# Optimization experiments

Hardware: AMD Instinct MI355X
Metric: run time of the kernel (lower is better)

The kernel has to match this reference:

```python
import jax, jax.numpy as jnp
import numpy as np

N, E, B = 100000, 640000, 2000
NODE_TYPES, EDGE_TYPES = 16, 5
ND, ED, EMB, L = 256, 128, 256, 3  # node_dim, edge_dim, emb_dim, num encoder blocks


def setup_inputs() -> dict:
    key = jax.random.key(0)
    ks = jax.random.split(key, 20)
    s = 0.02
    inp = {
        "h_node": jax.random.normal(ks[0], (N, NODE_TYPES), jnp.float32),
        "pos_node": jax.random.normal(ks[1], (N, 3), jnp.float32),
        "h_edge": jax.random.normal(ks[2], (E, EDGE_TYPES), jnp.float32),
        "W_node": jax.random.normal(ks[3], (NODE_TYPES, ND), jnp.float32) * s,
        "W_edge": jax.random.normal(ks[4], (EDGE_TYPES, ED), jnp.float32) * s,
        # per-block encoder params (stacked over L blocks)
        "W_eu": jax.random.normal(ks[5], (L, ED + 2 * ND + 1, ED), jnp.float32) * s,
        "b_eu": jnp.zeros((L, ED), jnp.float32),
        "W_msg": jax.random.normal(ks[6], (L, ND + ED, ND), jnp.float32) * s,
        "b_msg": jnp.zeros((L, ND), jnp.float32),
        "W_nu": jax.random.normal(ks[7], (L, 2 * ND, ND), jnp.float32) * s,
        "b_nu": jnp.zeros((L, ND), jnp.float32),
        # final MLP: in=ND+ED, hidden=2*EMB, out=EMB (num_layer=2)
        "Wf1": jax.random.normal(ks[8], (ND + ED, 2 * EMB), jnp.float32) * s,
        "bf1": jnp.zeros((2 * EMB,), jnp.float32),
        "Wf2": jax.random.normal(ks[9], (2 * EMB, EMB), jnp.float32) * s,
        "bf2": jnp.zeros((EMB,), jnp.float32),
        "edge_index": jax.random.randint(ks[10], (2, E), 0, N, jnp.int64),
        "batch_node": jnp.sort(jax.random.randint(ks[11], (N,), 0, B, jnp.int64)),
        "batch_edge": jnp.sort(jax.random.randint(ks[12], (E,), 0, B, jnp.int64)),
    }
    return inp


def _segment_mean(x, ids, num_segments):
    tot = jax.ops.segment_sum(x, ids, num_segments=num_segments)
    cnt = jax.ops.segment_sum(jnp.ones((x.shape[0], 1), x.dtype), ids,
                              num_segments=num_segments)
    return tot / jnp.maximum(cnt, 1.0)


def reference(h_node, pos_node, h_edge, W_node, W_edge, W_eu, b_eu,
              W_msg, b_msg, W_nu, b_nu, Wf1, bf1, Wf2, bf2,
              edge_index, batch_node, batch_edge):
    src, dst = edge_index[0], edge_index[1]
    # embed node / edge type features
    hn = h_node @ W_node            # [N, ND]
    he = h_edge @ W_edge            # [E, ED]
    # NodeEdgeNet: L message-passing blocks with geometric edge feature
    dist = jnp.linalg.norm(pos_node[dst] - pos_node[src], axis=-1,
                           keepdims=True)  # [E, 1]
    for l in range(L):
        e_in = jnp.concatenate([he, hn[src], hn[dst], dist], axis=-1)
        he = jax.nn.relu(e_in @ W_eu[l] + b_eu[l])                 # edge update
        msg = jax.nn.relu(jnp.concatenate([hn[src], he], axis=-1)
                          @ W_msg[l] + b_msg[l])                    # [E, ND]
        agg = jax.ops.segment_sum(msg, dst, num_segments=N)         # [N, ND]
        hn = hn + jax.nn.relu(jnp.concatenate([hn, agg], axis=-1)
                              @ W_nu[l] + b_nu[l])                  # node update
    # per-graph mean pooling (replaces python loop over k with segment mean)
    mean_n = _segment_mean(hn, batch_node, B)   # [B, ND]
    mean_e = _segment_mean(he, batch_edge, B)   # [B, ED]
    h_sub = jnp.concatenate([mean_n, mean_e], axis=-1)  # [B, ND+ED]
    emb = jax.nn.relu(h_sub @ Wf1 + bf1) @ Wf2 + bf2     # [B, EMB]
    return emb, batch_node
```

## Files before the change

kernel.cpp:

```cpp
#include <hip/hip_runtime.h>
#include <hip/hip_bf16.h>
#include <math.h>

#define NN 100000
#define NE 640000
#define NB 2000

typedef __attribute__((ext_vector_type(4))) float v4f;
typedef long long ll64;
#define MFMA8(a, b, c) __builtin_amdgcn_mfma_f32_16x16x32_fp8_fp8(a, b, c, 0, 0, 0)

#define INV_S 0.000244140625f
#define ASCL 16.0f
#define AINV 0.0625f

#if __has_builtin(__builtin_amdgcn_cvt_pk_fp8_f32) && __has_builtin(__builtin_amdgcn_cvt_f32_fp8)
#define HW_FP8 1
#else
#define HW_FP8 0
#endif

__device__ __forceinline__ int IDX(const void* p, size_t i, int is64) {
    return is64 ? (int)((const long long*)p)[i] : ((const int*)p)[i];
}
__device__ __forceinline__ int clampi(int v, int n) {
    return ((unsigned)v < (unsigned)n) ? v : 0;
}

__global__ void k_detect(const int* bn32, int* flag) {
    if (threadIdx.x == 0 && blockIdx.x == 0) {
        int is64 = 1;
        for (int k = 50001; k < 50401; k += 2)
            if (bn32[k] != 0) { is64 = 0; break; }
        *flag = is64;
    }
}

__device__ __forceinline__ unsigned sw_enc_fp8(float x) {
    unsigned s = (__float_as_uint(x) >> 24) & 0x80u;
    float ax = fminf(fabsf(x), 448.f);
    if (ax < 0.015625f) {
        unsigned m = (unsigned)(ax * 512.f + 0.5f);
        return s | m;
    }
    unsigned b = __float_as_uint(ax) + 0x00080000u;
    unsigned e = (b >> 23) - 120u;
    unsigned m = (b >> 20) & 7u;
    unsigned v = (e << 3) | m;
    if (v > 0x7Eu) v = 0x7Eu;
    return s | v;
}
__device__ __forceinline__ float sw_dec_fp8(unsigned b) {
    unsigned s = (b & 0x80u) << 24;
    unsigned e = (b >> 3) & 15u;
    unsigned m = b & 7u;
    if (e) return __uint_as_float(s | ((e + 120u) << 23) | (m << 20));
    float f = (float)m * 0.001953125f;
    return (b & 0x80u) ? -f : f;
}
__device__ __forceinline__ unsigned enc1(float x) {
#if HW_FP8
    return (unsigned)__builtin_amdgcn_cvt_pk_fp8_f32(x, x, 0, false) & 255u;
#else
    return sw_enc_fp8(x);
#endif
}
__device__ __forceinline__ unsigned encpk(float a, float b) {
#if HW_FP8
    return (unsigned)__builtin_amdgcn_cvt_pk_fp8_f32(a, b, 0, false) & 0xFFFFu;
#else
    return sw_enc_fp8(a) | (sw_enc_fp8(b) << 8);
#endif
}
__device__ __forceinline__ float dec1(unsigned b) {
#if HW_FP8
    return __builtin_amdgcn_cvt_f32_fp8((int)b, 0);
#else
    return sw_dec_fp8(b);
#endif
}
__device__ __forceinline__ float bf_f(unsigned short u) {
    return __uint_as_float((unsigned)u << 16);
}
__device__ __forceinline__ unsigned short f_to_bf(float x) {
    __hip_bfloat16 h = __float2bfloat16(x);
    return *(unsigned short*)&h;
}

__global__ __launch_bounds__(256) void k_node_embed(const float* __restrict__ h_node,
                                                    const float* __restrict__ W,
                                                    unsigned char* __restrict__ hn8) {
    __shared__ float sh[8][16];
    int t = threadIdx.x;
    int r0 = blockIdx.x * 8;
    if (t < 128) sh[t >> 4][t & 15] = h_node[r0 * 16 + t];
    float w[16];
#pragma unroll
    for (int k = 0; k < 16; ++k) w[k] = W[k * 256 + t];
    __syncthreads();
#pragma unroll
    for (int r = 0; r < 8; ++r) {
        float acc = 0.f;
#pragma unroll
        for (int k = 0; k < 16; ++k) acc += sh[r][k] * w[k];
        hn8[(size_t)(r0 + r) * 256 + t] = (unsigned char)enc1(ASCL * acc);
    }
}

__global__ __launch_bounds__(256) void k_edge_embed(const float* __restrict__ h_edge,
                                                    const float* __restrict__ W,
                                                    const int* __restrict__ perm,
                                                    unsigned char* __restrict__ he8) {
    __shared__ float sh[16][5];
    int t = threadIdx.x;
    int e0 = blockIdx.x * 16;
    if (t < 80) {
        int row = t / 5, col = t % 5;
        int e = perm[e0 + row];
        sh[row][col] = h_edge[(size_t)e * 5 + col];
    }
    int c = t & 127;
    int es = t >> 7;
    float w[5];
#pragma unroll
    for (int k = 0; k < 5; ++k) w[k] = W[k * 128 + c];
    __syncthreads();
#pragma unroll
    for (int e = 0; e < 8; ++e) {
        int ee = es * 8 + e;
        float acc = 0.f;
#pragma unroll
        for (int k = 0; k < 5; ++k) acc += sh[ee][k] * w[k];
        he8[(size_t)(e0 + ee) * 128 + c] = (unsigned char)enc1(ASCL * acc);
    }
}

__global__ __launch_bounds__(256) void k_tr_w1(const float* __restrict__ W,
                                               unsigned char* __restrict__ WT) {
    int i = blockIdx.x * 256 + threadIdx.x;
    if (i >= 3 * 128 * 128) return;
    int l = i / 16384, r = i % 16384;
    int n = r / 128, k = r % 128;
    WT[i] = (unsigned char)enc1(256.f * W[(size_t)l * 641 * 128 + (size_t)k * 128 + n]);
}
__global__ __launch_bounds__(256) void k_tr_w2(const float* __restrict__ W,
                                               unsigned char* __restrict__ WT) {
    int i = blockIdx.x * 256 + threadIdx.x;
    if (i >= 3 * 256 * 128) return;
    int l = i / 32768, r = i % 32768;
    int n = r / 128, k = r % 128;
    WT[i] = (unsigned char)enc1(256.f * W[(size_t)l * 384 * 256 + (size_t)(256 + k) * 256 + n]);
}
__global__ __launch_bounds__(256) void k_tr_nu(const float* __restrict__ W,
                                               unsigned char* __restrict__ WT) {
    int i = blockIdx.x * 256 + threadIdx.x;
    if (i >= 3 * 256 * 512) return;
    int l = i / 131072, r = i % 131072;
    int n = r / 512, k = r % 512;
    WT[i] = (unsigned char)enc1(256.f * W[(size_t)l * 512 * 256 + (size_t)k * 256 + n]);
}
__global__ __launch_bounds__(256) void k_tr_pre(const float* __restrict__ Weu,
                                                const float* __restrict__ Wmsg,
                                                unsigned char* __restrict__ WT) {
    int i = blockIdx.x * 256 + threadIdx.x;
    if (i >= 3 * 512 * 256) return;
    int l = i / 131072, r = i % 131072;
    int n = r / 256, k = r % 256;
    float w;
    if (n < 128)      w = Weu[(size_t)l * 641 * 128 + (size_t)(128 + k) * 128 + n];
    else if (n < 256) w = Weu[(size_t)l * 641 * 128 + (size_t)(384 + k) * 128 + (n - 128)];
    else              w = Wmsg[(size_t)l * 384 * 256 + (size_t)k * 256 + (n - 256)];
    WT[i] = (unsigned char)enc1(256.f * w);
}

__global__ __launch_bounds__(256) void k_hist(const void* __restrict__ ei,
                                              const int* __restrict__ flag,
                                              int* __restrict__ hist) {
    int e = blockIdx.x * 256 + threadIdx.x;
    if (e >= NE) return;
    int d = clampi(IDX(ei, (size_t)NE + e, *flag), NN);
    atomicAdd(&hist[d], 1);
}
__global__ __launch_bounds__(1024) void k_scan(const int* __restrict__ hist,
                                               int* __restrict__ rowptr) {
    __shared__ int part[1024];
    int t = threadIdx.x;
    const int C = 98;
    int s = 0;
    for (int j = 0; j < C; ++j) {
        int i = t * C + j;
        if (i < NN) s += hist[i];
    }
    part[t] = s;
    __syncthreads();
    if (t == 0) {
        int run = 0;
        for (int i = 0; i < 1024; ++i) { int v = part[i]; part[i] = run; run += v; }
    }
    __syncthreads();
    int run = part[t];
    for (int j = 0; j < C; ++j) {
        int i = t * C + j;
        if (i < NN) { rowptr[i] = run; run += hist[i]; }
    }
}
__global__ __launch_bounds__(256) void k_perm(const void* __restrict__ ei,
                                              const int* __restrict__ flag,
                                              const float* __restrict__ pos,
                                              int* __restrict__ cursor,
                                              int* __restrict__ perm,
                                              int* __restrict__ inv,
                                              int* __restrict__ srcs,
                                              int* __restrict__ dsts,
                                              float* __restrict__ dist_s) {
    int e = blockIdx.x * 256 + threadIdx.x;
    if (e >= NE) return;
    int is64 = *flag;
    int s = clampi(IDX(ei, (size_t)e, is64), NN);
    int d = clampi(IDX(ei, (size_t)NE + e, is64), NN);
    int p = atomicAdd(&cursor[d], 1);
    perm[p] = e;
    inv[e] = p;
    srcs[p] = s;
    dsts[p] = d;
    float dx = pos[d * 3 + 0] - pos[s * 3 + 0];
    float dy = pos[d * 3 + 1] - pos[s * 3 + 1];
    float dz = pos[d * 3 + 2] - pos[s * 3 + 2];
    dist_s[p] = sqrtf(dx * dx + dy * dy + dz * dz);
}

#define NP_AS 264
__global__ __launch_bounds__(256, 3) void k_node_pre(
    const unsigned char* __restrict__ hn8, const unsigned char* __restrict__ WpreT,
    unsigned char* __restrict__ R) {
    __shared__ unsigned char s_A[64 * NP_AS];
    int t = threadIdx.x;
    int rb = blockIdx.x * 64;
    {
        int row = t >> 2, sb = t & 3;
        int gr = rb + row; if (gr >= NN) gr = NN - 1;
        const uint4* sp = (const uint4*)(hn8 + (size_t)gr * 256 + sb * 64);
        uint4 a = sp[0], b = sp[1], c = sp[2], d = sp[3];
        uint4* dp = (uint4*)&s_A[row * NP_AS + sb * 64];
        dp[0] = a; dp[1] = b; dp[2] = c; dp[3] = d;
    }
    __syncthreads();
    int lane = t & 63, wv = t >> 6, quad = lane >> 4, l16 = lane & 15;
    v4f zero4 = {0.f, 0.f, 0.f, 0.f};
#pragma unroll
    for (int pass = 0; pass < 2; ++pass) {
        int nt0 = wv * 8 + pass * 4;
        v4f acc[4][4];
#pragma unroll
        for (int mt = 0; mt < 4; ++mt)
#pragma unroll
            for (int nl = 0; nl < 4; ++nl) acc[mt][nl] = zero4;
#pragma unroll 2
        for (int k = 0; k < 256; k += 32) {
            int ko = k + quad * 8;
            ll64 b[4];
#pragma unroll
            for (int nl = 0; nl < 4; ++nl)
                b[nl] = *(const ll64*)(WpreT + (size_t)((nt0 + nl) * 16 + l16) * 256 + ko);
#pragma unroll
            for (int mt = 0; mt < 4; ++mt) {
                ll64 a = *(const ll64*)&s_A[(mt * 16 + l16) * NP_AS + ko];
#pragma unroll
                for (int nl = 0; nl < 4; ++nl) acc[mt][nl] = MFMA8(a, b[nl], acc[mt][nl]);
            }
        }
#pragma unroll
        for (int nl = 0; nl < 4; ++nl) {
            int c = (nt0 + nl) * 16 + l16;
#pragma unroll
            for (int mt = 0; mt < 4; ++mt)
#pragma unroll
                for (int rr = 0; rr < 2; ++rr) {
                    int rw0 = mt * 16 + quad * 4 + rr * 2;
                    unsigned pk = encpk(acc[mt][nl][rr * 2] * 0.00390625f,
                                        acc[mt][nl][rr * 2 + 1] * 0.00390625f);
                    if (rb + rw0 < NN)
                        R[(size_t)(rb + rw0) * 512 + c] = (unsigned char)(pk & 255u);
                    if (rb + rw0 + 1 < NN)
                        R[(size_t)(rb + rw0 + 1) * 512 + c] = (unsigned char)(pk >> 8);
                }
        }
    }
}

#define EF_S 136
#define EF_QS 264
#define EF_MS 264
__global__ __launch_bounds__(256, 4) void k_edge_fused(
    unsigned char* __restrict__ he8, const unsigned char* __restrict__ R,
    const float* __restrict__ dist_s,
    const int* __restrict__ srcs, const int* __restrict__ dsts,
    const unsigned char* __restrict__ W1T, const float* __restrict__ W_eu,
    const float* __restrict__ b_eu,
    const unsigned char* __restrict__ W2T, const float* __restrict__ b_msg,
    unsigned short* __restrict__ agg) {
    __shared__ __align__(16) unsigned char s_A[32 * EF_S];
    __shared__ __align__(16) unsigned char s_Pd[32 * EF_S];
    __shared__ __align__(16) unsigned char s_Ph[32 * EF_S];
    __shared__ __align__(16) unsigned char s_Q[32 * EF_QS];
    __shared__ __align__(16) unsigned short s_msg[32 * EF_MS];
    __shared__ float s_dist[32];
    __shared__ int s_dsti[32];
    int t = threadIdx.x;
    int eb = blockIdx.x * 32;
    int row = t >> 3, sb = t & 7;
    int sid = srcs[eb + row];
    int did = dsts[eb + row];
    if (t < 32) {
        s_dsti[t] = dsts[eb + t];
        s_dist[t] = dist_s[eb + t];
    }
    *(uint4*)&s_A[row * EF_S + sb * 16] =
        *(const uint4*)(he8 + (size_t)(eb + row) * 128 + sb * 16);
    *(uint4*)&s_Ph[row * EF_S + sb * 16] =
        *(const uint4*)(R + (size_t)sid * 512 + sb * 16);
    *(uint4*)&s_Pd[row * EF_S + sb * 16] =
        *(const uint4*)(R + (size_t)did * 512 + 128 + sb * 16);
    {
        const uint4* qp = (const uint4*)(R + (size_t)sid * 512 + 256 + sb * 32);
        uint4 q0 = qp[0], q1 = qp[1];
        *(uint4*)&s_Q[row * EF_QS + sb * 32] = q0;
        *(uint4*)&s_Q[row * EF_QS + sb * 32 + 16] = q1;
    }
    int lane = t & 63, wv = t >> 6, quad = lane >> 4, l16 = lane & 15;
    int n0 = wv * 2;
    const unsigned char* B0 = W1T + (size_t)(n0 * 16 + l16) * 128 + quad * 8;
    ll64 Brg[4][2];
#pragma unroll
    for (int kk = 0; kk < 4; ++kk) {
        Brg[kk][0] = *(const ll64*)(B0 + kk * 32);
        Brg[kk][1] = *(const ll64*)(B0 + 2048 + kk * 32);
    }
    __syncthreads();

    v4f zero4 = {0.f, 0.f, 0.f, 0.f};
    v4f acc[2][2];
    acc[0][0] = zero4; acc[0][1] = zero4; acc[1][0] = zero4; acc[1][1] = zero4;
#pragma unroll
    for (int kk = 0; kk < 4; ++kk) {
        int ko = kk * 32 + quad * 8;
#pragma unroll
        for (int mt = 0; mt < 2; ++mt) {
            ll64 a = *(const ll64*)&s_A[(mt * 16 + l16) * EF_S + ko];
            acc[mt][0] = MFMA8(a, Brg[kk][0], acc[mt][0]);
            acc[mt][1] = MFMA8(a, Brg[kk][1], acc[mt][1]);
        }
    }
#pragma unroll
    for (int nl = 0; nl < 2; ++nl) {
        int c = (n0 + nl) * 16 + l16;
        float w640 = W_eu[640 * 128 + c];
        float bb = b_eu[c];
#pragma unroll
        for (int mt = 0; mt < 2; ++mt)
#pragma unroll
            for (int rr = 0; rr < 2; ++rr) {
                int rw0 = mt * 16 + quad * 4 + rr * 2;
                int rw1 = rw0 + 1;
                float S0 = (dec1(s_Ph[rw0 * EF_S + c]) +
                            dec1(s_Pd[rw0 * EF_S + c])) * AINV;
                float S1 = (dec1(s_Ph[rw1 * EF_S + c]) +
                            dec1(s_Pd[rw1 * EF_S + c])) * AINV;
                float v0 = fmaxf(acc[mt][nl][rr * 2] * INV_S + S0 +
                                 s_dist[rw0] * w640 + bb, 0.f);
                float v1 = fmaxf(acc[mt][nl][rr * 2 + 1] * INV_S + S1 +
                                 s_dist[rw1] * w640 + bb, 0.f);
                unsigned pk = encpk(ASCL * v0, ASCL * v1);
                unsigned char q0 = (unsigned char)(pk & 255u);
                unsigned char q1 = (unsigned char)(pk >> 8);
                s_Ph[rw0 * EF_S + c] = q0;
                s_Ph[rw1 * EF_S + c] = q1;
                he8[(size_t)(eb + rw0) * 128 + c] = q0;
                he8[(size_t)(eb + rw1) * 128 + c] = q1;
            }
    }
    __syncthreads();

    v4f mac[2][4];
#pragma unroll
    for (int nl = 0; nl < 4; ++nl) { mac[0][nl] = zero4; mac[1][nl] = zero4; }
    int q0n = wv * 4;
#pragma unroll
    for (int kk = 0; kk < 4; ++kk) {
        int ko = kk * 32 + quad * 8;
        ll64 b[4];
#pragma unroll
        for (int nl = 0; nl < 4; ++nl)
            b[nl] = *(const ll64*)(W2T + (size_t)((q0n + nl) * 16 + l16) * 128 + ko);
#pragma unroll
        for (int mt = 0; mt < 2; ++mt) {
            ll64 a = *(const ll64*)&s_Ph[(mt * 16 + l16) * EF_S + ko];
#pragma unroll
            for (int nl = 0; nl < 4; ++nl) mac[mt][nl] = MFMA8(a, b[nl], mac[mt][nl]);
        }
    }
#pragma unroll
    for (int nl = 0; nl < 4; ++nl) {
        int c = (q0n + nl) * 16 + l16;
        float bm = b_msg[c];
#pragma unroll
        for (int mt = 0; mt < 2; ++mt)
#pragma unroll
            for (int r = 0; r < 4; ++r) {
                int rw = mt * 16 + quad * 4 + r;
                float qv = dec1(s_Q[rw * EF_QS + c]) * AINV;
                float v = fmaxf(mac[mt][nl][r] * INV_S + qv + bm, 0.f);
                s_msg[rw * EF_MS + c] = f_to_bf(v);
            }
    }
    __syncthreads();
    {
        int cp = t & 127;
        int half = t >> 7;
        int r0 = half * 16, r1 = r0 + 16;
        float ax = 0.f, ay = 0.f;
        int cur = s_dsti[r0];
        for (int rw = r0; rw < r1; ++rw) {
            int d2 = s_dsti[rw];
            if (d2 != cur) {
                if (ax != 0.f || ay != 0.f) {
                    __hip_bfloat162 pv;
                    pv.x = __float2bfloat16(ax);
                    pv.y = __float2bfloat16(ay);
                    unsafeAtomicAdd((__hip_bfloat162*)&agg[(size_t)cur * 256 + cp * 2], pv);
                }
                ax = 0.f; ay = 0.f; cur = d2;
            }
            unsigned v = *(const unsigned*)&s_msg[rw * EF_MS + cp * 2];
            ax += bf_f((unsigned short)(v & 0xFFFFu));
            ay += bf_f((unsigned short)(v >> 16));
        }
        if (ax != 0.f || ay != 0.f) {
            __hip_bfloat162 pv;
            pv.x = __float2bfloat16(ax);
            pv.y = __float2bfloat16(ay);
            unsafeAtomicAdd((__hip_bfloat162*)&agg[(size_t)cur * 256 + cp * 2], pv);
        }
    }
}

#define NL_AS 520
__global__ __launch_bounds__(256, 3) void k_node_layer(
    unsigned char* __restrict__ hn8, const unsigned short* __restrict__ agg,
    const unsigned char* __restrict__ WnuT, const float* __restrict__ b) {
    __shared__ unsigned char s_A[64 * NL_AS];
    int t = threadIdx.x;
    int rb = blockIdx.x * 64;
    {
        int row = t >> 2, sb = t & 3;
        int gr = rb + row; if (gr >= NN) gr = NN - 1;
        const uint4* sp = (const uint4*)(hn8 + (size_t)gr * 256 + sb * 64);
        uint4 a = sp[0], b2 = sp[1], c = sp[2], d = sp[3];
        uint4* dp = (uint4*)&s_A[row * NL_AS + sb * 64];
        dp[0] = a; dp[1] = b2; dp[2] = c; dp[3] = d;
        const unsigned short* ap = agg + (size_t)gr * 256 + sb * 64;
        unsigned char* dq = &s_A[row * NL_AS + 256 + sb * 64];
#pragma unroll
        for (int j = 0; j < 64; j += 2) {
            unsigned pk = encpk(ASCL * bf_f(ap[j]), ASCL * bf_f(ap[j + 1]));
            *(unsigned short*)&dq[j] = (unsigned short)pk;
        }
    }
    __syncthreads();
    int lane = t & 63, wv = t >> 6, quad = lane >> 4, l16 = lane & 15;
    v4f zero4 = {0.f, 0.f, 0.f, 0.f};
    v4f acc[4][4];
#pragma unroll
    for (int mt = 0; mt < 4; ++mt)
#pragma unroll
        for (int nl = 0; nl < 4; ++nl) acc[mt][nl] = zero4;
    int q0 = wv * 4;
#pragma unroll 2
    for (int k = 0; k < 512; k += 32) {
        int ko = k + quad * 8;
        ll64 b2[4];
#pragma unroll
        for (int nl = 0; nl < 4; ++nl)
            b2[nl] = *(const ll64*)(WnuT + (size_t)((q0 + nl) * 16 + l16) * 512 + ko);
#pragma unroll
        for (int mt = 0; mt < 4; ++mt) {
            ll64 a = *(const ll64*)&s_A[(mt * 16 + l16) * NL_AS + ko];
#pragma unroll
            for (int nl = 0; nl < 4; ++nl) acc[mt][nl] = MFMA8(a, b2[nl], acc[mt][nl]);
        }
    }
#pragma unroll
    for (int nl = 0; nl < 4; ++nl) {
        int c = (q0 + nl) * 16 + l16;
        float bv = b[c];
#pragma unroll
        for (int mt = 0; mt < 4; ++mt)
#pragma unroll
            for (int rr = 0; rr < 2; ++rr) {
                int rw0 = mt * 16 + quad * 4 + rr * 2;
                float o0 = dec1(s_A[rw0 * NL_AS + c]) * AINV;
                float o1 = dec1(s_A[(rw0 + 1) * NL_AS + c]) * AINV;
                float v0 = o0 + fmaxf(acc[mt][nl][rr * 2] * INV_S + bv, 0.f);
                float v1 = o1 + fmaxf(acc[mt][nl][rr * 2 + 1] * INV_S + bv, 0.f);
                unsigned pk = encpk(ASCL * v0, ASCL * v1);
                if (rb + rw0 < NN)
                    hn8[(size_t)(rb + rw0) * 256 + c] = (unsigned char)(pk & 255u);
                if (rb + rw0 + 1 < NN)
                    hn8[(size_t)(rb + rw0 + 1) * 256 + c] = (unsigned char)(pk >> 8);
            }
    }
}

__device__ __forceinline__ int lbound(const void* a, int n, int v, int is64) {
    int lo = 0, hi = n;
    while (lo < hi) {
        int mid = (lo + hi) >> 1;
        if (IDX(a, mid, is64) < v) lo = mid + 1; else hi = mid;
    }
    return lo;
}

__global__ __launch_bounds__(512) void k_pool_mlp(
    const unsigned char* __restrict__ hn8, const unsigned char* __restrict__ he8,
    const int* __restrict__ inv,
    const void* __restrict__ bn, const void* __restrict__ be,
    const int* __restrict__ flag,
    const float* __restrict__ Wf1, const float* __restrict__ bf1,
    const float* __restrict__ Wf2, const float* __restrict__ bf2,
    float* __restrict__ out) {
    __shared__ float s_sub[384];
    __shared__ float s_hid[512];
    int b = blockIdx.x;
    int t = threadIdx.x;
    int is64 = *flag;
    if (t < 256) {
        int lo = lbound(bn, NN, b, is64), hi = lbound(bn, NN, b + 1, is64);
        float s = 0.f;
        for (int i = lo; i < hi; ++i) s += dec1(hn8[(size_t)i * 256 + t]);
        s_sub[t] = s * AINV / fmaxf((float)(hi - lo), 1.f);
    } else if (t < 384) {
        int c = t - 256;
        int lo = lbound(be, NE, b, is64), hi = lbound(be, NE, b + 1, is64);
        float s = 0.f;
        for (int i = lo; i < hi; ++i)
            s += dec1(he8[(size_t)inv[i] * 128 + c]);
        s_sub[256 + c] = s * AINV / fmaxf((float)(hi - lo), 1.f);
    }
    __syncthreads();
    float hacc = bf1[t];
    for (int k = 0; k < 384; ++k) hacc += s_sub[k] * Wf1[k * 512 + t];
    s_hid[t] = fmaxf(hacc, 0.f);
    __syncthreads();
    if (t < 256) {
        float o = bf2[t];
        for (int k = 0; k < 512; ++k) o += s_hid[k] * Wf2[k * 256 + t];
        out[(size_t)b * 256 + t] = o;
    }
}

__global__ __launch_bounds__(256) void k_write_batch(const void* __restrict__ bn,
                                                     const int* __restrict__ flag,
                                                     float* __restrict__ out) {
    int i = blockIdx.x * 256 + threadIdx.x;
    if (i < NN) out[(size_t)NB * 256 + i] = (float)IDX(bn, i, *flag);
}

__global__ __launch_bounds__(256) void k_fill(float* __restrict__ p, int n, float v) {
    int i = blockIdx.x * 256 + threadIdx.x;
    if (i < n) p[i] = v;
}

extern "C" void kernel_launch(void* const* d_in, const int* in_sizes, int n_in,
                              void* d_out, int out_size, void* d_ws, size_t ws_size,
                              hipStream_t stream) {
    const float* h_node = (const float*)d_in[0];
    const float* pos    = (const float*)d_in[1];
    const float* h_edge = (const float*)d_in[2];
    const float* W_node = (const float*)d_in[3];
    const float* W_edge = (const float*)d_in[4];
    const float* W_eu   = (const float*)d_in[5];
    const float* b_eu   = (const float*)d_in[6];
    const float* W_msg  = (const float*)d_in[7];
    const float* b_msg  = (const float*)d_in[8];
    const float* W_nu   = (const float*)d_in[9];
    const float* b_nu   = (const float*)d_in[10];
    const float* Wf1    = (const float*)d_in[11];
    const float* bf1    = (const float*)d_in[12];
    const float* Wf2    = (const float*)d_in[13];
    const float* bf2    = (const float*)d_in[14];
    const void* ei = d_in[15];
    const void* bn = d_in[16];
    const void* be = d_in[17];

    float* out = (float*)d_out;

    const size_t SZ_FLAG = 256;
    const size_t SZ_HN   = (size_t)NN * 256;
    const size_t SZ_HE   = (size_t)NE * 128;
    const size_t SZ_AGG  = (size_t)NN * 256 * 2;
    const size_t SZ_R    = (size_t)NN * 512;
    const size_t SZ_PERM = (size_t)NE * 4;
    const size_t SZ_INV  = (size_t)NE * 4;
    const size_t SZ_SRC  = (size_t)NE * 4;
    const size_t SZ_DST  = (size_t)NE * 4;
    const size_t SZ_DS   = (size_t)NE * 4;
    const size_t SZ_PTR  = 512 * 1024;
    const size_t SZ_CUR  = 512 * 1024;
    const size_t SZ_W1   = (size_t)3 * 128 * 128;
    const size_t SZ_W2   = (size_t)3 * 256 * 128;
    const size_t SZ_WNU  = (size_t)3 * 256 * 512;
    const size_t SZ_WPRE = (size_t)3 * 512 * 256;
    const size_t NEED = SZ_FLAG + SZ_HN + SZ_HE + SZ_AGG + SZ_R + SZ_PERM +
                        SZ_INV + SZ_SRC + SZ_DST + SZ_DS + SZ_PTR + SZ_CUR +
                        SZ_W1 + SZ_W2 + SZ_WNU + SZ_WPRE;

    char* ws = (char*)d_ws;
    int* flag = (int*)ws;                       ws += SZ_FLAG;
    unsigned char* hn8 = (unsigned char*)ws;    ws += SZ_HN;
    unsigned char* he8 = (unsigned char*)ws;    ws += SZ_HE;
    unsigned short* agg = (unsigned short*)ws;  ws += SZ_AGG;
    unsigned char* R = (unsigned char*)ws;      ws += SZ_R;
    int* perm = (int*)ws;                       ws += SZ_PERM;
    int* inv = (int*)ws;                        ws += SZ_INV;
    int* srcs = (int*)ws;                       ws += SZ_SRC;
    int* dsts = (int*)ws;                       ws += SZ_DST;
    float* dist_s = (float*)ws;                 ws += SZ_DS;
    int* rowptr = (int*)ws;                     ws += SZ_PTR;
    int* cursor = (int*)ws;                     ws += SZ_CUR;
    unsigned char* W1T = (unsigned char*)ws;    ws += SZ_W1;
    unsigned char* W2T = (unsigned char*)ws;    ws += SZ_W2;
    unsigned char* WnuT = (unsigned char*)ws;   ws += SZ_WNU;
    unsigned char* WpreT = (unsigned char*)ws;  ws += SZ_WPRE;

    if (ws_size < NEED) {
        float enc = -(100000.0f + (float)(ws_size >> 20));
        k_detect<<<1, 64, 0, stream>>>((const int*)bn, flag);
        k_fill<<<(NB * 256 + 255) / 256, 256, 0, stream>>>(out, NB * 256, enc);
        k_write_batch<<<(NN + 255) / 256, 256, 0, stream>>>(bn, flag, out);
        return;
    }

    k_detect<<<1, 64, 0, stream>>>((const int*)bn, flag);
    k_tr_w1<<<(3 * 128 * 128 + 255) / 256, 256, 0, stream>>>(W_eu, W1T);
    k_tr_w2<<<(3 * 256 * 128 + 255) / 256, 256, 0, stream>>>(W_msg, W2T);
    k_tr_nu<<<(3 * 256 * 512 + 255) / 256, 256, 0, stream>>>(W_nu, WnuT);
    k_tr_pre<<<(3 * 512 * 256 + 255) / 256, 256, 0, stream>>>(W_eu, W_msg, WpreT);
    k_node_embed<<<NN / 8, 256, 0, stream>>>(h_node, W_node, hn8);

    hipMemsetAsync(cursor, 0, (size_t)NN * 4, stream);
    k_hist<<<(NE + 255) / 256, 256, 0, stream>>>(ei, flag, cursor);
    k_scan<<<1, 1024, 0, stream>>>(cursor, rowptr);
    hipMemcpyAsync(cursor, rowptr, (size_t)NN * 4, hipMemcpyDeviceToDevice, stream);
    k_perm<<<(NE + 255) / 256, 256, 0, stream>>>(ei, flag, pos, cursor, perm,
                                                 inv, srcs, dsts, dist_s);
    k_edge_embed<<<NE / 16, 256, 0, stream>>>(h_edge, W_edge, perm, he8);

    for (int l = 0; l < 3; ++l) {
        hipMemsetAsync(agg, 0, SZ_AGG, stream);
        k_node_pre<<<(NN + 63) / 64, 256, 0, stream>>>(
            hn8, WpreT + (size_t)l * 512 * 256, R);
        k_edge_fused<<<NE / 32, 256, 0, stream>>>(
            he8, R, dist_s, srcs, dsts,
            W1T + (size_t)l * 128 * 128, W_eu + (size_t)l * 641 * 128,
            b_eu + (size_t)l * 128,
            W2T + (size_t)l * 256 * 128, b_msg + (size_t)l * 256, agg);
        k_node_layer<<<(NN + 63) / 64, 256, 0, stream>>>(
            hn8, agg, WnuT + (size_t)l * 256 * 512, b_nu + (size_t)l * 256);
    }

    k_pool_mlp<<<NB, 512, 0, stream>>>(hn8, he8, inv, bn, be, flag,
                                       Wf1, bf1, Wf2, bf2, out);
    k_write_batch<<<(NN + 255) / 256, 256, 0, stream>>>(bn, flag, out);
}
```

Measured before the change: 1.931 ms.

## Fuse next-layer node projection into node update; parallelize pooling across warps

The node-update kernel now keeps its freshly quantized output rows in shared memory and immediately computes the next layer's per-node projection R from them. This removes the separate k_node_pre launch and its re-read of hn8 for layers two and three. It adds a second LDS buffer, which may reduce occupancy. Separately, the pooling kernel now has all 8 waves stride over nodes and edges with 4-byte vector loads and reduces partial sums in shared memory, instead of one thread per column walking each segment serially.

```diff
diff --git a/kernel.cpp b/kernel.cpp
--- a/kernel.cpp
+++ b/kernel.cpp
@@ -444,11 +444,15 @@
     }
 }
 
-#define NL_AS 520
-__global__ __launch_bounds__(256, 3) void k_node_layer(
+#define NF_AS 520
+#define NF_BS 264
+__global__ __launch_bounds__(256, 3) void k_node_fused(
     unsigned char* __restrict__ hn8, const unsigned short* __restrict__ agg,
-    const unsigned char* __restrict__ WnuT, const float* __restrict__ b) {
-    __shared__ unsigned char s_A[64 * NL_AS];
+    const unsigned char* __restrict__ WnuT, const float* __restrict__ b,
+    const unsigned char* __restrict__ WpreT, unsigned char* __restrict__ R,
+    int do_pre) {
+    __shared__ unsigned char s_A[64 * NF_AS];
+    __shared__ unsigned char s_B[64 * NF_BS];
     int t = threadIdx.x;
     int rb = blockIdx.x * 64;
     {
@@ -456,10 +460,10 @@
         int gr = rb + row; if (gr >= NN) gr = NN - 1;
         const uint4* sp = (const uint4*)(hn8 + (size_t)gr * 256 + sb * 64);
         uint4 a = sp[0], b2 = sp[1], c = sp[2], d = sp[3];
-        uint4* dp = (uint4*)&s_A[row * NL_AS + sb * 64];
+        uint4* dp = (uint4*)&s_A[row * NF_AS + sb * 64];
         dp[0] = a; dp[1] = b2; dp[2] = c; dp[3] = d;
         const unsigned short* ap = agg + (size_t)gr * 256 + sb * 64;
-        unsigned char* dq = &s_A[row * NL_AS + 256 + sb * 64];
+        unsigned char* dq = &s_A[row * NF_AS + 256 + sb * 64];
 #pragma unroll
         for (int j = 0; j < 64; j += 2) {
             unsigned pk = encpk(ASCL * bf_f(ap[j]), ASCL * bf_f(ap[j + 1]));
@@ -469,45 +473,92 @@
     __syncthreads();
     int lane = t & 63, wv = t >> 6, quad = lane >> 4, l16 = lane & 15;
     v4f zero4 = {0.f, 0.f, 0.f, 0.f};
-    v4f acc[4][4];
-#pragma unroll
-    for (int mt = 0; mt < 4; ++mt)
-#pragma unroll
-        for (int nl = 0; nl < 4; ++nl) acc[mt][nl] = zero4;
-    int q0 = wv * 4;
+    {
+        v4f acc[4][4];
+#pragma unroll
+        for (int mt = 0; mt < 4; ++mt)
+#pragma unroll
+            for (int nl = 0; nl < 4; ++nl) acc[mt][nl] = zero4;
+        int q0 = wv * 4;
 #pragma unroll 2
-    for (int k = 0; k < 512; k += 32) {
-        int ko = k + quad * 8;
-        ll64 b2[4];
-#pragma unroll
-        for (int nl = 0; nl < 4; ++nl)
-            b2[nl] = *(const ll64*)(WnuT + (size_t)((q0 + nl) * 16 + l16) * 512 + ko);
-#pragma unroll
-        for (int mt = 0; mt < 4; ++mt) {
-            ll64 a = *(const ll64*)&s_A[(mt * 16 + l16) * NL_AS + ko];
-#pragma unroll
-            for (int nl = 0; nl < 4; ++nl) acc[mt][nl] = MFMA8(a, b2[nl], acc[mt][nl]);
-        }
-    }
-#pragma unroll
-    for (int nl = 0; nl < 4; ++nl) {
-        int c = (q0 + nl) * 16 + l16;
-        float bv = b[c];
+        for (int k = 0; k < 512; k += 32) {
+            int ko = k + quad * 8;
+            ll64 b2[4];
+#pragma unroll
+            for (int nl = 0; nl < 4; ++nl)
+                b2[nl] = *(const ll64*)(WnuT + (size_t)((q0 + nl) * 16 + l16) * 512 + ko);
+#pragma unroll
+            for (int mt = 0; mt < 4; ++mt) {
+                ll64 a = *(const ll64*)&s_A[(mt * 16 + l16) * NF_AS + ko];
+#pragma unroll
+                for (int nl = 0; nl < 4; ++nl) acc[mt][nl] = MFMA8(a, b2[nl], acc[mt][nl]);
+            }
+        }
+#pragma unroll
+        for (int nl = 0; nl < 4; ++nl) {
+            int c = (q0 + nl) * 16 + l16;
+            float bv = b[c];
+#pragma unroll
+            for (int mt = 0; mt < 4; ++mt)
+#pragma unroll
+                for (int rr = 0; rr < 2; ++rr) {
+                    int rw0 = mt * 16 + quad * 4 + rr * 2;
+                    float o0 = dec1(s_A[rw0 * NF_AS + c]) * AINV;
+                    float o1 = dec1(s_A[(rw0 + 1) * NF_AS + c]) * AINV;
+                    float v0 = o0 + fmaxf(acc[mt][nl][rr * 2] * INV_S + bv, 0.f);
+                    float v1 = o1 + fmaxf(acc[mt][nl][rr * 2 + 1] * INV_S + bv, 0.f);
+                    unsigned pk = encpk(ASCL * v0, ASCL * v1);
+                    unsigned char q0b = (unsigned char)(pk & 255u);
+                    unsigned char q1b = (unsigned char)(pk >> 8);
+                    s_B[rw0 * NF_BS + c] = q0b;
+                    s_B[(rw0 + 1) * NF_BS + c] = q1b;
+                    if (rb + rw0 < NN)
+                        hn8[(size_t)(rb + rw0) * 256 + c] = q0b;
+                    if (rb + rw0 + 1 < NN)
+                        hn8[(size_t)(rb + rw0 + 1) * 256 + c] = q1b;
+                }
+        }
+    }
+    if (!do_pre) return;
+    __syncthreads();
+#pragma unroll
+    for (int pass = 0; pass < 2; ++pass) {
+        int nt0 = wv * 8 + pass * 4;
+        v4f acc[4][4];
 #pragma unroll
         for (int mt = 0; mt < 4; ++mt)
 #pragma unroll
-            for (int rr = 0; rr < 2; ++rr) {
-                int rw0 = mt * 16 + quad * 4 + rr * 2;
-                float o0 = dec1(s_A[rw0 * NL_AS + c]) * AINV;
-                float o1 = dec1(s_A[(rw0 + 1) * NL_AS + c]) * AINV;
-                float v0 = o0 + fmaxf(acc[mt][nl][rr * 2] * INV_S + bv, 0.f);
-                float v1 = o1 + fmaxf(acc[mt][nl][rr * 2 + 1] * INV_S + bv, 0.f);
-                unsigned pk = encpk(ASCL * v0, ASCL * v1);
-                if (rb + rw0 < NN)
-                    hn8[(size_t)(rb + rw0) * 256 + c] = (unsigned char)(pk & 255u);
-                if (rb + rw0 + 1 < NN)
-                    hn8[(size_t)(rb + rw0 + 1) * 256 + c] = (unsigned char)(pk >> 8);
+            for (int nl = 0; nl < 4; ++nl) acc[mt][nl] = zero4;
+#pragma unroll 2
+        for (int k = 0; k < 256; k += 32) {
+            int ko = k + quad * 8;
+            ll64 b2[4];
+#pragma unroll
+            for (int nl = 0; nl < 4; ++nl)
+                b2[nl] = *(const ll64*)(WpreT + (size_t)((nt0 + nl) * 16 + l16) * 256 + ko);
+#pragma unroll
+            for (int mt = 0; mt < 4; ++mt) {
+                ll64 a = *(const ll64*)&s_B[(mt * 16 + l16) * NF_BS + ko];
+#pragma unroll
+                for (int nl = 0; nl < 4; ++nl) acc[mt][nl] = MFMA8(a, b2[nl], acc[mt][nl]);
             }
+        }
+#pragma unroll
+        for (int nl = 0; nl < 4; ++nl) {
+            int c = (nt0 + nl) * 16 + l16;
+#pragma unroll
+            for (int mt = 0; mt < 4; ++mt)
+#pragma unroll
+                for (int rr = 0; rr < 2; ++rr) {
+                    int rw0 = mt * 16 + quad * 4 + rr * 2;
+                    unsigned pk = encpk(acc[mt][nl][rr * 2] * 0.00390625f,
+                                        acc[mt][nl][rr * 2 + 1] * 0.00390625f);
+                    if (rb + rw0 < NN)
+                        R[(size_t)(rb + rw0) * 512 + c] = (unsigned char)(pk & 255u);
+                    if (rb + rw0 + 1 < NN)
+                        R[(size_t)(rb + rw0 + 1) * 512 + c] = (unsigned char)(pk >> 8);
+                }
+        }
     }
 }
 
@@ -528,23 +579,59 @@
     const float* __restrict__ Wf1, const float* __restrict__ bf1,
     const float* __restrict__ Wf2, const float* __restrict__ bf2,
     float* __restrict__ out) {
+    __shared__ float s_nacc[8][256];
+    __shared__ float s_eacc[16][128];
     __shared__ float s_sub[384];
     __shared__ float s_hid[512];
     int b = blockIdx.x;
     int t = threadIdx.x;
     int is64 = *flag;
+    int lane = t & 63, wv = t >> 6;
+    int nlo = lbound(bn, NN, b, is64), nhi = lbound(bn, NN, b + 1, is64);
+    int elo = lbound(be, NE, b, is64), ehi = lbound(be, NE, b + 1, is64);
+    {
+        float a0 = 0.f, a1 = 0.f, a2 = 0.f, a3 = 0.f;
+        for (int i = nlo + wv; i < nhi; i += 8) {
+            unsigned u = *(const unsigned*)(hn8 + (size_t)i * 256 + lane * 4);
+            a0 += dec1(u & 255u);
+            a1 += dec1((u >> 8) & 255u);
+            a2 += dec1((u >> 16) & 255u);
+            a3 += dec1(u >> 24);
+        }
+        s_nacc[wv][lane * 4 + 0] = a0;
+        s_nacc[wv][lane * 4 + 1] = a1;
+        s_nacc[wv][lane * 4 + 2] = a2;
+        s_nacc[wv][lane * 4 + 3] = a3;
+    }
+    {
+        int g16 = wv * 2 + (lane >> 5);
+        int sl = lane & 31;
+        float a0 = 0.f, a1 = 0.f, a2 = 0.f, a3 = 0.f;
+        for (int e = elo + g16; e < ehi; e += 16) {
+            int row = inv[e];
+            unsigned u = *(const unsigned*)(he8 + (size_t)row * 128 + sl * 4);
+            a0 += dec1(u & 255u);
+            a1 += dec1((u >> 8) & 255u);
+            a2 += dec1((u >> 16) & 255u);
+            a3 += dec1(u >> 24);
+        }
+        s_eacc[g16][sl * 4 + 0] = a0;
+        s_eacc[g16][sl * 4 + 1] = a1;
+        s_eacc[g16][sl * 4 + 2] = a2;
+        s_eacc[g16][sl * 4 + 3] = a3;
+    }
+    __syncthreads();
     if (t < 256) {
-        int lo = lbound(bn, NN, b, is64), hi = lbound(bn, NN, b + 1, is64);
         float s = 0.f;
-        for (int i = lo; i < hi; ++i) s += dec1(hn8[(size_t)i * 256 + t]);
-        s_sub[t] = s * AINV / fmaxf((float)(hi - lo), 1.f);
+#pragma unroll
+        for (int w = 0; w < 8; ++w) s += s_nacc[w][t];
+        s_sub[t] = s * AINV / fmaxf((float)(nhi - nlo), 1.f);
     } else if (t < 384) {
         int c = t - 256;
-        int lo = lbound(be, NE, b, is64), hi = lbound(be, NE, b + 1, is64);
         float s = 0.f;
-        for (int i = lo; i < hi; ++i)
-            s += dec1(he8[(size_t)inv[i] * 128 + c]);
-        s_sub[256 + c] = s * AINV / fmaxf((float)(hi - lo), 1.f);
+#pragma unroll
+        for (int j = 0; j < 16; ++j) s += s_eacc[j][c];
+        s_sub[t] = s * AINV / fmaxf((float)(ehi - elo), 1.f);
     }
     __syncthreads();
     float hacc = bf1[t];
@@ -655,17 +742,20 @@
                                                  inv, srcs, dsts, dist_s);
     k_edge_embed<<<NE / 16, 256, 0, stream>>>(h_edge, W_edge, perm, he8);
 
+    k_node_pre<<<(NN + 63) / 64, 256, 0, stream>>>(hn8, WpreT, R);
+
     for (int l = 0; l < 3; ++l) {
         hipMemsetAsync(agg, 0, SZ_AGG, stream);
-        k_node_pre<<<(NN + 63) / 64, 256, 0, stream>>>(
-            hn8, WpreT + (size_t)l * 512 * 256, R);
         k_edge_fused<<<NE / 32, 256, 0, stream>>>(
             he8, R, dist_s, srcs, dsts,
             W1T + (size_t)l * 128 * 128, W_eu + (size_t)l * 641 * 128,
             b_eu + (size_t)l * 128,
             W2T + (size_t)l * 256 * 128, b_msg + (size_t)l * 256, agg);
-        k_node_layer<<<(NN + 63) / 64, 256, 0, stream>>>(
-            hn8, agg, WnuT + (size_t)l * 256 * 512, b_nu + (size_t)l * 256);
+        int do_pre = (l < 2) ? 1 : 0;
+        const unsigned char* wpre_next = WpreT + (size_t)(do_pre ? (l + 1) : 0) * 512 * 256;
+        k_node_fused<<<(NN + 63) / 64, 256, 0, stream>>>(
+            hn8, agg, WnuT + (size_t)l * 256 * 512, b_nu + (size_t)l * 256,
+            wpre_next, R, do_pre);
     }
 
     k_pool_mlp<<<NB, 512, 0, stream>>>(hn8, he8, inv, bn, be, flag,
```

After: 1.776 ms. 8.0% less time.
